# Performance work log

Hardware: AMD Instinct MI355X
Metric: run time of the kernel (lower is better)

The kernel has to match this reference:

```python
import jax, jax.numpy as jnp
import numpy as np

THRESH = 0.5
DECAY = 0.2

B = 16384
IN_DIM = 784
HID = 400
OUT = 10


def act_fun(mem):
    # spike = (mem > thresh).float()
    return (mem > THRESH).astype(mem.dtype)


def setup_inputs() -> dict:
    key = jax.random.key(0)
    kx, k1, k2, k3, k4 = jax.random.split(key, 5)
    x = jax.random.uniform(kx, (B, IN_DIM), dtype=jnp.float32)  # pixel probs in [0,1]
    W1 = jax.random.normal(k1, (HID, IN_DIM), dtype=jnp.float32) * (1.0 / np.sqrt(IN_DIM))
    b1 = jax.random.normal(k2, (HID,), dtype=jnp.float32) * 0.01
    W2 = jax.random.normal(k3, (OUT, HID), dtype=jnp.float32) * (1.0 / np.sqrt(HID))
    b2 = jax.random.normal(k4, (OUT,), dtype=jnp.float32) * 0.01
    return {"x": x, "W1": W1, "b1": b1, "W2": W2, "b2": b2, "time_window": 20}


def reference(x, W1, b1, W2, b2, time_window):
    Bsz = x.shape[0]
    keys = jax.random.split(jax.random.key(42), time_window)

    def step(carry, k):
        h1_mem, h1_spike, h2_mem, h2_spike, h2_sum = carry
        u = jax.random.uniform(k, x.shape, dtype=x.dtype)
        xi = (x > u).astype(x.dtype)  # Bernoulli spike encoding of input
        # LIF layer 1
        h1_mem = h1_mem * DECAY * (1.0 - h1_spike) + xi @ W1.T + b1
        h1_spike = act_fun(h1_mem)
        # LIF layer 2
        h2_mem = h2_mem * DECAY * (1.0 - h2_spike) + h1_spike @ W2.T + b2
        h2_spike = act_fun(h2_mem)
        return (h1_mem, h1_spike, h2_mem, h2_spike, h2_sum + h2_spike), None

    z_h = jnp.zeros((Bsz, HID), dtype=x.dtype)
    z_o = jnp.zeros((Bsz, OUT), dtype=x.dtype)
    init = (z_h, z_h, z_o, z_o, z_o)
    (_, _, _, _, h2_sum), _ = jax.lax.scan(step, init, keys)
    return h2_sum / time_window
```

## Files before the change

kernel.cpp:

```cpp
#include <hip/hip_runtime.h>
#include <stdint.h>


#define INDIM  784
#define HID    400
#define ODIM   10
#define TSTEPS 20
#define NS     16384

#define KW     25
#define NCOL   416
#define NB_N   13
#define BROWG  202
#define BROWL  203
#define MS     256
#define NLIMB  5

#define XI_DW   ((size_t)TSTEPS * NS * KW)
#define SPK_OFF (XI_DW)
#define SPK_DW  ((size_t)NS * TSTEPS * NB_N)
#define BL_OFF  (XI_DW + SPK_DW)
#define WS_NEED ((XI_DW + SPK_DW + (size_t)NLIMB * NCOL * BROWG) * 4)

#define TD   8
#define NT   98
#define WTJ  512
#define XIW  26
#define SPW  14

typedef int i32x4  __attribute__((ext_vector_type(4)));
typedef int i32x16 __attribute__((ext_vector_type(16)));

__device__ __forceinline__ void tfr(uint32_t& x0, uint32_t& x1, int r) {
  x0 += x1;
  x1 = (x1 << r) | (x1 >> (32 - r));
  x1 ^= x0;
}

__device__ __forceinline__ uint2 tf2x32(uint32_t k0, uint32_t k1,
                                        uint32_t c0, uint32_t c1) {
  uint32_t k2 = k0 ^ k1 ^ 0x1BD11BDAu;
  uint32_t x0 = c0 + k0, x1 = c1 + k1;
  tfr(x0,x1,13); tfr(x0,x1,15); tfr(x0,x1,26); tfr(x0,x1,6);
  x0 += k1; x1 += k2 + 1u;
  tfr(x0,x1,17); tfr(x0,x1,29); tfr(x0,x1,16); tfr(x0,x1,24);
  x0 += k2; x1 += k0 + 2u;
  tfr(x0,x1,13); tfr(x0,x1,15); tfr(x0,x1,26); tfr(x0,x1,6);
  x0 += k0; x1 += k1 + 3u;
  tfr(x0,x1,17); tfr(x0,x1,29); tfr(x0,x1,16); tfr(x0,x1,24);
  x0 += k1; x1 += k2 + 4u;
  tfr(x0,x1,13); tfr(x0,x1,15); tfr(x0,x1,26); tfr(x0,x1,6);
  x0 += k2; x1 += k0 + 5u;
  return make_uint2(x0, x1);
}

__device__ __forceinline__ float bits_to_unif(uint32_t b) {
  return __uint_as_float((b >> 9) | 0x3f800000u) - 1.0f;
}


__global__ __launch_bounds__(256, 4)
void snn_prep(const float* __restrict__ x, const float* __restrict__ W1,
              uint32_t* __restrict__ ws) {
  const int tid = threadIdx.x, bid = blockIdx.x;
  if (bid < 4096) {
    const int wv = tid >> 6, lane = tid & 63;
    const int s  = bid * 4 + wv;
    float xv[13];
#pragma unroll
    for (int c = 0; c < 13; ++c) {
      const int d = c * 64 + lane;
      xv[c] = (d < INDIM) ? x[s * INDIM + d] : 0.0f;
    }
    for (int t = 0; t < TSTEPS; ++t) {
      const uint2 kt = tf2x32(0u, 42u, 0u, (uint32_t)t);
      uint32_t* dst = ws + ((size_t)t * NS + s) * KW;
#pragma unroll
      for (int c = 0; c < 13; ++c) {
        const int d = c * 64 + lane;
        int xb = 0;
        if (d < INDIM) {
          uint2 r = tf2x32(kt.x, kt.y, 0u, (uint32_t)(s * INDIM + d));
          xb = xv[c] > bits_to_unif(r.x ^ r.y);
        }
        unsigned long long m = __ballot(xb);
        if (lane == 0) {
          dst[2*c] = (uint32_t)m;
          if (2*c + 1 < KW) dst[2*c + 1] = (uint32_t)(m >> 32);
        }
      }
    }
  } else {
    const int idx = (bid - 4096) * 256 + tid;
    if (idx < NCOL * BROWG) {
      const int col = idx / BROWG, grp = idx - col * BROWG;
      uint32_t dw[NLIMB] = {0u, 0u, 0u, 0u, 0u};
#pragma unroll
      for (int b = 0; b < 4; ++b) {
        const int d = grp * 4 + b;
        double w = 0.0;
        if (col < HID && d < INDIM) w = (double)W1[col * INDIM + d];
        long long V = (long long)rint(w * 0x1p41);
        const long long CAP = 547599908735ll;
        if (V >  CAP) V =  CAP;
        if (V < -CAP) V = -CAP;
#pragma unroll
        for (int l = 0; l < NLIMB; ++l) {
          const int r = (int)(((V + 128) & 255) - 128);
          dw[l] |= ((uint32_t)(uint8_t)(int8_t)r) << (8 * b);
          V = (V - r) >> 8;
        }
      }
      uint32_t* bl = ws + BL_OFF;
#pragma unroll
      for (int l = 0; l < NLIMB; ++l)
        bl[((size_t)l * NCOL + col) * BROWG + grp] = dw[l];
    }
  }
}

__global__ __launch_bounds__(256, 1)
void snn_l1(const float* __restrict__ b1, uint32_t* __restrict__ ws) {
  __shared__ uint32_t blds[NLIMB][32 * BROWL];
  __shared__ uint32_t xi_lds[MS * KW];
  __shared__ uint32_t spkbuf[MS];

  const int tid = threadIdx.x;
  const int bid = blockIdx.x;
  const int x8  = bid & 7;
  const int q   = bid >> 3;
  const int nb  = q % NB_N;
  const int mb  = x8 + 8 * (q / NB_N);
  const int n0  = nb * 32, sbase = mb * MS;
  const int wv  = tid >> 6, lane = tid & 63;
  const int half = lane >> 5, c31 = lane & 31;
  const int col = n0 + c31;
  const double bb = (col < HID) ? (double)b1[col] : 0.0;

  const uint32_t* xi_ws  = ws;
  uint32_t*       spk_ws = ws + SPK_OFF;
  const uint32_t* bl_ws  = ws + BL_OFF;

  for (int i = tid; i < NLIMB * 32 * BROWG; i += 256) {
    const int l  = i / (32 * BROWG);
    const int r  = i - l * (32 * BROWG);
    const int c  = r / BROWG;
    const int gd = r - c * BROWG;
    blds[l][c * BROWL + gd] =
        bl_ws[((size_t)l * NCOL + n0 + c) * BROWG + gd];
  }
  {
    const uint32_t* src = xi_ws + ((size_t)0 * NS + sbase) * KW;
#pragma unroll
    for (int j = 0; j < KW; ++j)
      xi_lds[tid + j * 256] = src[tid + j * 256];
  }
  uint32_t pf[KW];
  {
    const uint32_t* src = xi_ws + ((size_t)1 * NS + sbase) * KW;
#pragma unroll
    for (int j = 0; j < KW; ++j) pf[j] = src[tid + j * 256];
  }
  __syncthreads();

  double mem[2][16];
  uint32_t sp[2] = {0u, 0u};
#pragma unroll
  for (int T = 0; T < 2; ++T)
#pragma unroll
    for (int i = 0; i < 16; ++i) mem[T][i] = 0.0;

  const uint32_t* xr0 = &xi_lds[(wv * 64 +  0 + c31) * KW];
  const uint32_t* xr1 = &xi_lds[(wv * 64 + 32 + c31) * KW];
  const uint32_t* bb0 = &blds[0][c31 * BROWL + half * 4];

  for (int t = 0; t < TSTEPS; ++t) {
#pragma unroll
    for (int T = 0; T < 2; ++T)
#pragma unroll
      for (int i = 0; i < 16; ++i)
        mem[T][i] = ((sp[T] >> i) & 1u) ? 0.0 : mem[T][i] * 0.2;

    i32x16 acc[NLIMB][2];
#pragma unroll
    for (int l = 0; l < NLIMB; ++l)
#pragma unroll
      for (int T = 0; T < 2; ++T)
#pragma unroll
        for (int i = 0; i < 16; ++i) acc[l][T][i] = 0;

#pragma unroll 5
    for (int ks = 0; ks < 25; ++ks) {
      const uint32_t hw0 = (xr0[ks] >> (16 * half)) & 0xFFFFu;
      const uint32_t hw1 = (xr1[ks] >> (16 * half)) & 0xFFFFu;
      i32x4 a0, a1;
#pragma unroll
      for (int qq = 0; qq < 4; ++qq) {
        a0[qq] = (int)((((hw0 >> (4*qq)) & 0xFu) * 0x00204081u) & 0x01010101u);
        a1[qq] = (int)((((hw1 >> (4*qq)) & 0xFu) * 0x00204081u) & 0x01010101u);
      }
#pragma unroll
      for (int l = 0; l < NLIMB; ++l) {
        const uint32_t* bp = bb0 + l * (32 * BROWL) + ks * 8;
        const uint2 p0 = *(const uint2*)(bp);
        const uint2 p1 = *(const uint2*)(bp + 2);
        i32x4 bfr;
        bfr[0] = (int)p0.x; bfr[1] = (int)p0.y;
        bfr[2] = (int)p1.x; bfr[3] = (int)p1.y;
        acc[l][0] = __builtin_amdgcn_mfma_i32_32x32x32_i8(a0, bfr, acc[l][0],
                                                          0, 0, 0);
        acc[l][1] = __builtin_amdgcn_mfma_i32_32x32x32_i8(a1, bfr, acc[l][1],
                                                          0, 0, 0);
      }
    }

    double sc = 0x1p-41;
#pragma unroll
    for (int l = 0; l < NLIMB; ++l) {
#pragma unroll
      for (int i = 0; i < 16; ++i) {
        mem[0][i] += (double)acc[l][0][i] * sc;
        mem[1][i] += (double)acc[l][1][i] * sc;
      }
      sc *= 256.0;
    }

    uint32_t m0 = 0u, m1 = 0u;
#pragma unroll
    for (int i = 0; i < 16; ++i) {
      mem[0][i] += bb;  if (mem[0][i] > 0.5) m0 |= (1u << i);
      mem[1][i] += bb;  if (mem[1][i] > 0.5) m1 |= (1u << i);
    }
    sp[0] = m0; sp[1] = m1;

#pragma unroll
    for (int T = 0; T < 2; ++T) {
      const uint32_t mm = T ? m1 : m0;
#pragma unroll
      for (int rg = 0; rg < 16; ++rg) {
        unsigned long long bm = __ballot((mm >> rg) & 1u);
        if (lane == 0) {
          const int rlo = (rg & 3) + 8 * (rg >> 2);
          const int sl  = wv * 64 + T * 32 + rlo;
          spkbuf[sl]     = (uint32_t)bm;
          spkbuf[sl + 4] = (uint32_t)(bm >> 32);
        }
      }
    }
    __syncthreads();

    spk_ws[((size_t)nb * TSTEPS + t) * NS + sbase + tid] = spkbuf[tid];

    if (t + 1 < TSTEPS) {
#pragma unroll
      for (int j = 0; j < KW; ++j) xi_lds[tid + j * 256] = pf[j];
      const int tn = (t + 2 < TSTEPS) ? t + 2 : TSTEPS - 1;
      const uint32_t* src = xi_ws + ((size_t)tn * NS + sbase) * KW;
#pragma unroll
      for (int j = 0; j < KW; ++j) pf[j] = src[tid + j * 256];
      __syncthreads();
    }
  }
}

__global__ __launch_bounds__(256, 4)
void snn_l2(const float* __restrict__ W2, const float* __restrict__ b2,
            const uint32_t* __restrict__ ws, float* __restrict__ out) {
  const int gid    = blockIdx.x * 256 + threadIdx.x;
  const int sample = gid / ODIM;
  const int oc     = gid - sample * ODIM;
  const uint32_t* spk_ws = ws + SPK_OFF;

  double m2 = 0.0; int s2 = 0, cnt2 = 0;
  const double b2r = (double)b2[oc];
  const float4* w2p = (const float4*)(W2 + oc * HID);

  for (int t = 0; t < TSTEPS; ++t) {
    uint32_t sw[NB_N];
#pragma unroll
    for (int w = 0; w < NB_N; ++w)
      sw[w] = spk_ws[((size_t)w * TSTEPS + t) * NS + sample];
    sw[12] &= 0xFFFFu;

    const double a2 = s2 ? 0.0 : m2 * 0.2;
    double d0 = 0.0, d1 = 0.0, d2 = 0.0, d3 = 0.0;
#pragma unroll 2
    for (int w = 0; w < 12; ++w) {
      const uint32_t word = sw[w];
#pragma unroll
      for (int qq = 0; qq < 8; ++qq) {
        const float4 v4 = w2p[8 * w + qq];
        const uint32_t nib = (word >> (4 * qq)) & 0xFu;
        d0 = fma((double)v4.x, (double)(nib & 1u),        d0);
        d1 = fma((double)v4.y, (double)((nib >> 1) & 1u), d1);
        d2 = fma((double)v4.z, (double)((nib >> 2) & 1u), d2);
        d3 = fma((double)v4.w, (double)((nib >> 3) & 1u), d3);
      }
    }
    {
      const uint32_t word = sw[12];
#pragma unroll
      for (int qq = 0; qq < 4; ++qq) {
        const float4 v4 = w2p[96 + qq];
        const uint32_t nib = (word >> (4 * qq)) & 0xFu;
        d0 = fma((double)v4.x, (double)(nib & 1u),        d0);
        d1 = fma((double)v4.y, (double)((nib >> 1) & 1u), d1);
        d2 = fma((double)v4.z, (double)((nib >> 2) & 1u), d2);
        d3 = fma((double)v4.w, (double)((nib >> 3) & 1u), d3);
      }
    }
    m2 = (a2 + ((d0 + d1) + (d2 + d3))) + b2r;
    s2 = (m2 > 0.5) ? 1 : 0;
    cnt2 += s2;
  }
  out[sample * ODIM + oc] = (float)((double)cnt2 / 20.0);
}

__global__ __launch_bounds__(512, 4)
void snn_fused_v6(const float* __restrict__ x,  const float* __restrict__ W1,
                  const float* __restrict__ b1, const float* __restrict__ W2,
                  const float* __restrict__ b2, float* __restrict__ out) {
  __shared__ double   wt[2][TD * WTJ];
  __shared__ uint32_t xib[2][16][XIW];
  __shared__ uint32_t spk[2][16][SPW];

  const int tid  = threadIdx.x;
  const int g    = blockIdx.x;
  const int wv   = tid >> 6;
  const int sg   = wv >> 1;
  const int kh   = wv & 1;
  const int lane = tid & 63;
  const int jb   = 256 * kh + lane;

  for (int i = tid; i < 2 * TD * WTJ; i += 512)
    if ((i & (WTJ - 1)) >= HID) (&wt[0][0])[i] = 0.0;

  double bb[4];
#pragma unroll
  for (int k = 0; k < 4; ++k) {
    const int j = jb + 64 * k;
    bb[k] = (j < HID) ? (double)b1[j] : 0.0;
  }

  double   mem1[4][4];
  double   acc1[4][4];
  uint32_t spv[4];
#pragma unroll
  for (int s = 0; s < 4; ++s) {
    spv[s] = 0u;
#pragma unroll
    for (int k = 0; k < 4; ++k) { mem1[s][k] = 0.0; acc1[s][k] = 0.0; }
  }

  const int ls = tid / ODIM;
  const int lo = tid - ls * ODIM;
  double m2 = 0.0;
  int    s2 = 0, cnt2 = 0;
  const double b2r = (tid < 160) ? (double)b2[lo] : 0.0;

  auto layer2_step = [&](int tt) {
    if (tid < 160) {
      double a2 = s2 ? 0.0 : m2 * 0.2;
      double d0 = 0.0, d1 = 0.0, d2 = 0.0, d3 = 0.0;
      const float4* w2p = (const float4*)(W2 + lo * HID);
#pragma unroll 4
      for (int qq = 0; qq < 100; ++qq) {
        const uint32_t nib = (spk[tt][ls][qq >> 3] >> ((qq & 7) * 4)) & 0xFu;
        const float4 v4 = w2p[qq];
        d0 = fma((double)v4.x, (double)(nib & 1u),        d0);
        d1 = fma((double)v4.y, (double)((nib >> 1) & 1u), d1);
        d2 = fma((double)v4.z, (double)((nib >> 2) & 1u), d2);
        d3 = fma((double)v4.w, (double)((nib >> 3) & 1u), d3);
      }
      m2 = (a2 + ((d0 + d1) + (d2 + d3))) + b2r;
      s2 = (m2 > 0.5) ? 1 : 0;
      cnt2 += s2;
    }
  };

  const bool stager = (tid < HID);
  float4 va = make_float4(0,0,0,0), vb = va;
  if (stager) {
    const float4* s0 = (const float4*)(W1 + tid * INDIM);
    va = s0[0]; vb = s0[1];
    double* dst = &wt[0][tid];
    dst[0*WTJ] = (double)va.x;  dst[1*WTJ] = (double)va.y;
    dst[2*WTJ] = (double)va.z;  dst[3*WTJ] = (double)va.w;
    dst[4*WTJ] = (double)vb.x;  dst[5*WTJ] = (double)vb.y;
    dst[6*WTJ] = (double)vb.z;  dst[7*WTJ] = (double)vb.w;
    const float4* s1 = (const float4*)(W1 + tid * INDIM + TD);
    va = s1[0]; vb = s1[1];
  }
  int cur = 0;
  int ld  = 2;
  __syncthreads();

  for (int tp = 0; tp < TSTEPS / 2; ++tp) {
    const uint2 ka = tf2x32(0u, 42u, 0u, (uint32_t)(2 * tp));
    const uint2 kb = tf2x32(0u, 42u, 0u, (uint32_t)(2 * tp + 1));
    const uint32_t kx[2] = { ka.x, kb.x };
    const uint32_t ky[2] = { ka.y, kb.y };

    const int cA = kh ? 7 : 0;
    const int cB = kh ? 13 : 7;
    for (int s = 0; s < 4; ++s) {
      const int q   = 4 * sg + s;
      const int row = g * 8 + (q & 7) + ((q >= 8) ? 8192 : 0);
      for (int c = cA; c < cB; ++c) {
        const int d = c * 64 + lane;
        const bool valid = (d < INDIM);
        float xv = 0.0f;
        if (valid) xv = x[row * INDIM + d];
        const uint32_t e = (uint32_t)row * (uint32_t)INDIM + (uint32_t)d;
#pragma unroll
        for (int tt = 0; tt < 2; ++tt) {
          int xb = 0;
          if (valid) {
            uint2 r = tf2x32(kx[tt], ky[tt], 0u, e);
            xb = xv > bits_to_unif(r.x ^ r.y);
          }
          unsigned long long m = __ballot(xb);
          if (lane == 0) {
            xib[tt][q][2*c]     = (uint32_t)m;
            xib[tt][q][2*c + 1] = (uint32_t)(m >> 32);
          }
        }
      }
    }
    __syncthreads();

#pragma unroll
    for (int s = 0; s < 4; ++s)
#pragma unroll
      for (int k = 0; k < 4; ++k) {
        mem1[s][k] = ((spv[s] >> k) & 1u) ? 0.0 : mem1[s][k] * 0.2;
        acc1[s][k] = 0.0;
      }

    for (int td = 0; td < NT; ++td) {
      if (stager) {
        double* dst = &wt[cur ^ 1][tid];
        dst[0*WTJ] = (double)va.x;  dst[1*WTJ] = (double)va.y;
        dst[2*WTJ] = (double)va.z;  dst[3*WTJ] = (double)va.w;
        dst[4*WTJ] = (double)vb.x;  dst[5*WTJ] = (double)vb.y;
        dst[6*WTJ] = (double)vb.z;  dst[7*WTJ] = (double)vb.w;
        const float4* src = (const float4*)(W1 + tid * INDIM + ld * TD);
        va = src[0]; vb = src[1];
      }
      ld = (ld + 1 == NT) ? 0 : ld + 1;

      const int wi = td >> 2, sh = (td & 3) * 8;
      uint32_t bA[4], bB[4];
#pragma unroll
      for (int s = 0; s < 4; ++s) {
        bA[s] = (uint32_t)__builtin_amdgcn_readfirstlane(
                  (int)((xib[0][4*sg + s][wi] >> sh) & 0xFFu));
        bB[s] = (uint32_t)__builtin_amdgcn_readfirstlane(
                  (int)((xib[1][4*sg + s][wi] >> sh) & 0xFFu));
      }

      const double* wp = &wt[cur][jb];
#pragma unroll
      for (int dt = 0; dt < TD; ++dt) {
        double wd[4];
#pragma unroll
        for (int k = 0; k < 4; ++k)
          wd[k] = wp[dt * WTJ + 64 * k];
#pragma unroll
        for (int s = 0; s < 4; ++s) {
          if (bA[s] & (1u << dt)) {
#pragma unroll
            for (int k = 0; k < 4; ++k) mem1[s][k] += wd[k];
          }
          if (bB[s] & (1u << dt)) {
#pragma unroll
            for (int k = 0; k < 4; ++k) acc1[s][k] += wd[k];
          }
        }
      }

      __syncthreads();
      cur ^= 1;
    }

#pragma unroll
    for (int s = 0; s < 4; ++s) {
      uint32_t m = 0u;
#pragma unroll
      for (int k = 0; k < 4; ++k) {
        mem1[s][k] += bb[k];
        if (mem1[s][k] > 0.5) m |= (1u << k);
      }
      spv[s] = m;
#pragma unroll
      for (int k = 0; k < 4; ++k) {
        unsigned long long bm = __ballot((m >> k) & 1u);
        const int w0 = 8 * kh + 2 * k;
        if (lane == 0 && w0 < SPW) {
          spk[0][4*sg + s][w0]     = (uint32_t)bm;
          spk[0][4*sg + s][w0 + 1] = (uint32_t)(bm >> 32);
        }
      }
    }

#pragma unroll
    for (int s = 0; s < 4; ++s) {
      uint32_t m = 0u;
#pragma unroll
      for (int k = 0; k < 4; ++k) {
        double v = ((spv[s] >> k) & 1u) ? 0.0 : mem1[s][k] * 0.2;
        v += acc1[s][k];
        v += bb[k];
        mem1[s][k] = v;
        if (v > 0.5) m |= (1u << k);
      }
      spv[s] = m;
#pragma unroll
      for (int k = 0; k < 4; ++k) {
        unsigned long long bm = __ballot((m >> k) & 1u);
        const int w0 = 8 * kh + 2 * k;
        if (lane == 0 && w0 < SPW) {
          spk[1][4*sg + s][w0]     = (uint32_t)bm;
          spk[1][4*sg + s][w0 + 1] = (uint32_t)(bm >> 32);
        }
      }
    }
    __syncthreads();

    layer2_step(0);
    layer2_step(1);
  }

  if (tid < 160) {
    const int row = g * 8 + (ls & 7) + ((ls >= 8) ? 8192 : 0);
    out[row * ODIM + lo] = (float)((double)cnt2 / 20.0);
  }
}

extern "C" void kernel_launch(void* const* d_in, const int* in_sizes, int n_in,
                              void* d_out, int out_size, void* d_ws, size_t ws_size,
                              hipStream_t stream) {
  const float* x  = (const float*)d_in[0];
  const float* W1 = (const float*)d_in[1];
  const float* b1 = (const float*)d_in[2];
  const float* W2 = (const float*)d_in[3];
  const float* b2 = (const float*)d_in[4];
  float* out = (float*)d_out;

  if (d_ws != nullptr && ws_size >= WS_NEED) {
    uint32_t* ws = (uint32_t*)d_ws;
    hipLaunchKernelGGL(snn_prep, dim3(4096 + 329), dim3(256), 0, stream,
                       x, W1, ws);
    hipLaunchKernelGGL(snn_l1, dim3(8 * NB_N * 8), dim3(256), 0, stream,
                       b1, ws);
    hipLaunchKernelGGL(snn_l2, dim3(640), dim3(256), 0, stream, W2, b2, ws, out);
  } else {
    hipLaunchKernelGGL(snn_fused_v6, dim3(1024), dim3(512), 0, stream,
                       x, W1, b1, W2, b2, out);
  }
}
```

Before: 3.477 ms.

## Split layer-1 MFMA work across 8 waves with padded LDS rows

The layer-1 kernel now runs 512 threads per block with 8 waves, each handling 32 samples instead of 64. This halves the per-thread accumulators and membrane state, freeing registers so two blocks can share a CU. The xi LDS rows are padded from 25 to 28 words, and the register prefetch of the next timestep is dropped in favour of a direct synchronous reload into LDS. The risk is that the next timestep's global loads are no longer hidden behind compute, and each wave reads each B fragment for only one MFMA instead of two, so B-operand reuse drops.

```diff
diff --git a/kernel.cpp b/kernel.cpp
--- a/kernel.cpp
+++ b/kernel.cpp
@@ -9,6 +9,7 @@
 #define NS     16384
 
 #define KW     25
+#define KWL    28
 #define NCOL   416
 #define NB_N   13
 #define BROWG  202
@@ -119,10 +120,10 @@
   }
 }
 
-__global__ __launch_bounds__(256, 1)
+__global__ __launch_bounds__(512, 2)
 void snn_l1(const float* __restrict__ b1, uint32_t* __restrict__ ws) {
   __shared__ uint32_t blds[NLIMB][32 * BROWL];
-  __shared__ uint32_t xi_lds[MS * KW];
+  __shared__ uint32_t xi_lds[MS * KWL];
   __shared__ uint32_t spkbuf[MS];
 
   const int tid = threadIdx.x;
@@ -141,7 +142,7 @@
   uint32_t*       spk_ws = ws + SPK_OFF;
   const uint32_t* bl_ws  = ws + BL_OFF;
 
-  for (int i = tid; i < NLIMB * 32 * BROWG; i += 256) {
+  for (int i = tid; i < NLIMB * 32 * BROWG; i += 512) {
     const int l  = i / (32 * BROWG);
     const int r  = i - l * (32 * BROWG);
     const int c  = r / BROWG;
@@ -151,66 +152,53 @@
   }
   {
     const uint32_t* src = xi_ws + ((size_t)0 * NS + sbase) * KW;
-#pragma unroll
-    for (int j = 0; j < KW; ++j)
-      xi_lds[tid + j * 256] = src[tid + j * 256];
-  }
-  uint32_t pf[KW];
-  {
-    const uint32_t* src = xi_ws + ((size_t)1 * NS + sbase) * KW;
-#pragma unroll
-    for (int j = 0; j < KW; ++j) pf[j] = src[tid + j * 256];
+    for (int idx = tid; idx < MS * KW; idx += 512) {
+      const int s = idx / KW, w = idx - s * KW;
+      xi_lds[s * KWL + w] = src[idx];
+    }
   }
   __syncthreads();
 
-  double mem[2][16];
-  uint32_t sp[2] = {0u, 0u};
-#pragma unroll
-  for (int T = 0; T < 2; ++T)
-#pragma unroll
-    for (int i = 0; i < 16; ++i) mem[T][i] = 0.0;
-
-  const uint32_t* xr0 = &xi_lds[(wv * 64 +  0 + c31) * KW];
-  const uint32_t* xr1 = &xi_lds[(wv * 64 + 32 + c31) * KW];
-  const uint32_t* bb0 = &blds[0][c31 * BROWL + half * 4];
+  double mem[16];
+  uint32_t sp = 0u;
+#pragma unroll
+  for (int i = 0; i < 16; ++i) mem[i] = 0.0;
+
+  const uint32_t* xr  = &xi_lds[(wv * 32 + c31) * KWL];
+  const uint32_t* bp0 = &blds[0][c31 * BROWL + half * 4];
 
   for (int t = 0; t < TSTEPS; ++t) {
 #pragma unroll
-    for (int T = 0; T < 2; ++T)
-#pragma unroll
-      for (int i = 0; i < 16; ++i)
-        mem[T][i] = ((sp[T] >> i) & 1u) ? 0.0 : mem[T][i] * 0.2;
-
-    i32x16 acc[NLIMB][2];
+    for (int i = 0; i < 16; ++i)
+      mem[i] = ((sp >> i) & 1u) ? 0.0 : mem[i] * 0.2;
+
+    uint32_t xw[KW];
+#pragma unroll
+    for (int j = 0; j < KW; ++j) xw[j] = xr[j];
+
+    i32x16 acc[NLIMB];
 #pragma unroll
     for (int l = 0; l < NLIMB; ++l)
 #pragma unroll
-      for (int T = 0; T < 2; ++T)
-#pragma unroll
-        for (int i = 0; i < 16; ++i) acc[l][T][i] = 0;
-
-#pragma unroll 5
-    for (int ks = 0; ks < 25; ++ks) {
-      const uint32_t hw0 = (xr0[ks] >> (16 * half)) & 0xFFFFu;
-      const uint32_t hw1 = (xr1[ks] >> (16 * half)) & 0xFFFFu;
-      i32x4 a0, a1;
-#pragma unroll
-      for (int qq = 0; qq < 4; ++qq) {
-        a0[qq] = (int)((((hw0 >> (4*qq)) & 0xFu) * 0x00204081u) & 0x01010101u);
-        a1[qq] = (int)((((hw1 >> (4*qq)) & 0xFu) * 0x00204081u) & 0x01010101u);
-      }
+      for (int i = 0; i < 16; ++i) acc[l][i] = 0;
+
+#pragma unroll
+    for (int ks = 0; ks < KW; ++ks) {
+      const uint32_t hw = (xw[ks] >> (16 * half)) & 0xFFFFu;
+      i32x4 a;
+#pragma unroll
+      for (int qq = 0; qq < 4; ++qq)
+        a[qq] = (int)((((hw >> (4*qq)) & 0xFu) * 0x00204081u) & 0x01010101u);
 #pragma unroll
       for (int l = 0; l < NLIMB; ++l) {
-        const uint32_t* bp = bb0 + l * (32 * BROWL) + ks * 8;
+        const uint32_t* bp = bp0 + l * (32 * BROWL) + ks * 8;
         const uint2 p0 = *(const uint2*)(bp);
         const uint2 p1 = *(const uint2*)(bp + 2);
         i32x4 bfr;
         bfr[0] = (int)p0.x; bfr[1] = (int)p0.y;
         bfr[2] = (int)p1.x; bfr[3] = (int)p1.y;
-        acc[l][0] = __builtin_amdgcn_mfma_i32_32x32x32_i8(a0, bfr, acc[l][0],
-                                                          0, 0, 0);
-        acc[l][1] = __builtin_amdgcn_mfma_i32_32x32x32_i8(a1, bfr, acc[l][1],
-                                                          0, 0, 0);
+        acc[l] = __builtin_amdgcn_mfma_i32_32x32x32_i8(a, bfr, acc[l],
+                                                       0, 0, 0);
       }
     }
 
@@ -218,46 +206,43 @@
 #pragma unroll
     for (int l = 0; l < NLIMB; ++l) {
 #pragma unroll
-      for (int i = 0; i < 16; ++i) {
-        mem[0][i] += (double)acc[l][0][i] * sc;
-        mem[1][i] += (double)acc[l][1][i] * sc;
-      }
+      for (int i = 0; i < 16; ++i)
+        mem[i] += (double)acc[l][i] * sc;
       sc *= 256.0;
     }
 
-    uint32_t m0 = 0u, m1 = 0u;
+    uint32_t m = 0u;
 #pragma unroll
     for (int i = 0; i < 16; ++i) {
-      mem[0][i] += bb;  if (mem[0][i] > 0.5) m0 |= (1u << i);
-      mem[1][i] += bb;  if (mem[1][i] > 0.5) m1 |= (1u << i);
-    }
-    sp[0] = m0; sp[1] = m1;
-
-#pragma unroll
-    for (int T = 0; T < 2; ++T) {
-      const uint32_t mm = T ? m1 : m0;
-#pragma unroll
-      for (int rg = 0; rg < 16; ++rg) {
-        unsigned long long bm = __ballot((mm >> rg) & 1u);
-        if (lane == 0) {
-          const int rlo = (rg & 3) + 8 * (rg >> 2);
-          const int sl  = wv * 64 + T * 32 + rlo;
-          spkbuf[sl]     = (uint32_t)bm;
-          spkbuf[sl + 4] = (uint32_t)(bm >> 32);
-        }
+      mem[i] += bb;
+      if (mem[i] > 0.5) m |= (1u << i);
+    }
+    sp = m;
+
+#pragma unroll
+    for (int rg = 0; rg < 16; ++rg) {
+      unsigned long long bm = __ballot((m >> rg) & 1u);
+      if (lane == 0) {
+        const int rlo = (rg & 3) + 8 * (rg >> 2);
+        spkbuf[wv * 32 + rlo]     = (uint32_t)bm;
+        spkbuf[wv * 32 + rlo + 4] = (uint32_t)(bm >> 32);
       }
     }
     __syncthreads();
 
-    spk_ws[((size_t)nb * TSTEPS + t) * NS + sbase + tid] = spkbuf[tid];
+    if (tid < MS)
+      spk_ws[((size_t)nb * TSTEPS + t) * NS + sbase + tid] = spkbuf[tid];
 
     if (t + 1 < TSTEPS) {
-#pragma unroll
-      for (int j = 0; j < KW; ++j) xi_lds[tid + j * 256] = pf[j];
-      const int tn = (t + 2 < TSTEPS) ? t + 2 : TSTEPS - 1;
-      const uint32_t* src = xi_ws + ((size_t)tn * NS + sbase) * KW;
-#pragma unroll
-      for (int j = 0; j < KW; ++j) pf[j] = src[tid + j * 256];
+      const uint32_t* src = xi_ws + ((size_t)(t + 1) * NS + sbase) * KW;
+#pragma unroll
+      for (int j = 0; j < 13; ++j) {
+        const int idx = tid + j * 512;
+        if (idx < MS * KW) {
+          const int s = idx / KW, w = idx - s * KW;
+          xi_lds[s * KWL + w] = src[idx];
+        }
+      }
       __syncthreads();
     }
   }
@@ -551,7 +536,7 @@
     uint32_t* ws = (uint32_t*)d_ws;
     hipLaunchKernelGGL(snn_prep, dim3(4096 + 329), dim3(256), 0, stream,
                        x, W1, ws);
-    hipLaunchKernelGGL(snn_l1, dim3(8 * NB_N * 8), dim3(256), 0, stream,
+    hipLaunchKernelGGL(snn_l1, dim3(8 * NB_N * 8), dim3(512), 0, stream,
                        b1, ws);
     hipLaunchKernelGGL(snn_l2, dim3(640), dim3(256), 0, stream, W2, b2, ws, out);
   } else {
```

New measurement: 5.543 ms. 59.4% more time.
